# Performance work log

Hardware: AMD Instinct MI355X
Metric: run time of the kernel (lower is better)

Reference implementation:

```python
import jax, jax.numpy as jnp
import numpy as np

N_NODES = 62      # config.note_num (SEED EEG electrodes)
BATCH   = 1024    # graphs per batch
IN_CH   = 5
HID     = 64
OUT_CH  = 3
K_HOPS  = 2       # config.K


def setup_inputs() -> dict:
    key = jax.random.key(0)
    ks = jax.random.split(key, 8)
    total = BATCH * N_NODES
    x = jax.random.normal(ks[0], (total, IN_CH), dtype=jnp.float32)
    # fully-connected per-graph edge_index in row-major order (incl. self-loops),
    # matching edge_weight.reshape(-1).repeat(batch_size) in the torch code
    src = jnp.repeat(jnp.arange(N_NODES, dtype=jnp.int32), N_NODES)
    dst = jnp.tile(jnp.arange(N_NODES, dtype=jnp.int32), N_NODES)
    offs = (jnp.arange(BATCH, dtype=jnp.int32) * N_NODES)[:, None]
    edge_index = jnp.stack([
        (src[None, :] + offs).reshape(-1),
        (dst[None, :] + offs).reshape(-1),
    ])  # [2, BATCH*3844]
    batch = jnp.repeat(jnp.arange(BATCH, dtype=jnp.int32), N_NODES)
    n_tril = N_NODES * (N_NODES + 1) // 2  # 1953
    edge_weight_param = jax.random.normal(ks[1], (n_tril,), dtype=jnp.float32)
    w1 = jax.random.normal(ks[2], (HID, IN_CH), dtype=jnp.float32) * (1.0 / np.sqrt(IN_CH))
    b1 = jnp.zeros((HID,), dtype=jnp.float32)
    w2 = jax.random.normal(ks[3], (HID, HID), dtype=jnp.float32) * (1.0 / np.sqrt(HID))
    b2 = jnp.zeros((HID,), dtype=jnp.float32)
    wfc = jax.random.normal(ks[4], (OUT_CH, HID), dtype=jnp.float32) * (1.0 / np.sqrt(HID))
    bfc = jnp.zeros((OUT_CH,), dtype=jnp.float32)
    return dict(x=x, edge_index=edge_index, batch=batch,
                edge_weight_param=edge_weight_param,
                w1=w1, b1=b1, w2=w2, b2=b2, wfc=wfc, bfc=bfc)


def _gcn_norm(edge_index, edge_weight, num_nodes):
    # Graph already contains every self-loop, so add_remaining_self_loops only
    # reorders edges; normalization math is identical on the original edge set.
    row, col = edge_index[0], edge_index[1]
    deg = jax.ops.segment_sum(jnp.abs(edge_weight), row, num_segments=num_nodes)
    deg_inv_sqrt = jnp.where(deg > 0, jax.lax.rsqrt(deg), 0.0)
    return deg_inv_sqrt[row] * edge_weight * deg_inv_sqrt[col]


def _rsgconv(x, src, dst, norm, w, b):
    n = x.shape[0]
    for _ in range(K_HOPS):  # K propagation hops (gather-scale-scatter)
        x = jax.ops.segment_sum(norm[:, None] * x[src], dst, num_segments=n)
    return x @ w.T + b


def reference(x, edge_index, batch, edge_weight_param, w1, b1, w2, b2, wfc, bfc):
    num_nodes = x.shape[0]
    # rebuild symmetric dense 62x62 edge-weight matrix from learnable tril vector
    xs, ys = jnp.tril_indices(N_NODES)
    W = jnp.zeros((N_NODES, N_NODES), dtype=x.dtype).at[xs, ys].set(edge_weight_param)
    W = W + W.T - jnp.diag(jnp.diag(W))
    edge_weight = jnp.tile(W.reshape(-1), BATCH)  # [BATCH*3844]
    norm = _gcn_norm(edge_index, edge_weight, num_nodes)
    src, dst = edge_index[0], edge_index[1]
    h = jax.nn.relu(_rsgconv(x, src, dst, norm, w1, b1))
    h = jax.nn.relu(_rsgconv(h, src, dst, norm, w2, b2))
    pooled = jax.ops.segment_sum(h, batch, num_segments=BATCH)  # global_add_pool
    # dropout is identity in eval mode
    return pooled @ wfc.T + bfc
```

## Files before the change

kernel.cpp:

```cpp
#include <hip/hip_runtime.h>

#define NN 62
#define NP 64
#define NBATCH 1024
#define IN_CH 5
#define HID 64
#define OUT_CH 3
#define NTRIL 1953
#define H1S 72
#define GS 17
#define SAS 68

typedef _Float16 f16;
typedef f16 half8 __attribute__((ext_vector_type(8)));
typedef float floatx4 __attribute__((ext_vector_type(4)));

__global__ __launch_bounds__(256, 4) void graph_net(
    const float* __restrict__ x,
    const float* __restrict__ ewp,
    const float* __restrict__ w1, const float* __restrict__ b1,
    const float* __restrict__ w2, const float* __restrict__ b2,
    const float* __restrict__ wfc, const float* __restrict__ bfc,
    float* __restrict__ out) {
    __shared__ __align__(16) char smem[37120];
    f16* sAh = (f16*)smem;
    f16* sAl = (f16*)(smem + 9216);
    f16* sUTh = (f16*)smem;
    f16* sUTl = (f16*)(smem + 9216);
    float* sG = (float*)smem;
    float* sA = (float*)(smem + 18432);
    f16* sA2h = (f16*)(smem + 18432);
    f16* sA2l = (f16*)(smem + 27648);
    f16* sH1h = (f16*)(smem + 18432);
    f16* sH1l = (f16*)(smem + 27648);
    float* sDinv = (float*)(smem + 36864);
    float* sPool = (float*)(smem + 36864);

    const int t = threadIdx.x;
    const int lane = t & 63;
    const int w = __builtin_amdgcn_readfirstlane(t >> 6);
    const int g = blockIdx.x;
    const float* xg = x + (size_t)g * (NN * IN_CH);

    const int jn = lane & 15;
    const int qd = lane >> 4;
    const int jglob = 16 * w + jn;

    int xi[IN_CH];
    {
        const int L = (lane < NN) ? lane : (NN - 1);
        const int* xgi = (const int*)xg;
#pragma unroll
        for (int c = 0; c < IN_CH; ++c) xi[c] = xgi[L * IN_CH + c];
    }
    float w1r[IN_CH];
#pragma unroll
    for (int c = 0; c < IN_CH; ++c) w1r[c] = w1[lane * IN_CH + c];

#pragma unroll
    for (int k = 0; k < 8; ++k) {
        int i = t + 256 * k;
        if (i < NTRIL) {
            int r = (int)((sqrtf(8.f * (float)i + 1.f) - 1.f) * 0.5f);
            while (r * (r + 1) / 2 > i) --r;
            while ((r + 1) * (r + 2) / 2 <= i) ++r;
            int c = i - r * (r + 1) / 2;
            float v = ewp[i];
            sA[r * SAS + c] = v;
            sA[c * SAS + r] = v;
        }
    }
    __syncthreads();

    if (t < NN) {
        float s0 = 0.f, s1 = 0.f;
        for (int j = 0; j < NN; j += 2) {
            s0 += fabsf(sA[t * SAS + j]);
            s1 += fabsf(sA[t * SAS + j + 1]);
        }
        float s = s0 + s1;
        sDinv[t] = (s > 0.f) ? (1.0f / sqrtf(s)) : 0.f;
    }
    __syncthreads();

#pragma unroll
    for (int k = 0; k < 16; ++k) {
        int idx = t + 256 * k;
        int r = idx >> 6, c = idx & 63;
        float v = (r < NN && c < NN) ? sDinv[r] * sA[r * SAS + c] * sDinv[c] : 0.f;
        f16 vh = (f16)v;
        sAh[r * H1S + c] = vh;
        sAl[r * H1S + c] = (f16)(v - (float)vh);
    }
    __syncthreads();

    half8 bSh[2], bSl[2];
#pragma unroll
    for (int ks = 0; ks < 2; ++ks) {
        bSh[ks] = *(const half8*)(sAh + jglob * H1S + qd * 8 + 32 * ks);
        bSl[ks] = *(const half8*)(sAl + jglob * H1S + qd * 8 + 32 * ks);
    }
    floatx4 D2[4];
#pragma unroll
    for (int T = 0; T < 4; ++T) { D2[T][0]=0.f; D2[T][1]=0.f; D2[T][2]=0.f; D2[T][3]=0.f; }
#pragma unroll
    for (int T = 0; T < 4; ++T) {
#pragma unroll
        for (int ks = 0; ks < 2; ++ks) {
            const half8 ah = *(const half8*)(sAh + (16 * T + jn) * H1S + qd * 8 + 32 * ks);
            const half8 al = *(const half8*)(sAl + (16 * T + jn) * H1S + qd * 8 + 32 * ks);
            D2[T] = __builtin_amdgcn_mfma_f32_16x16x32_f16(al, bSh[ks], D2[T], 0, 0, 0);
            D2[T] = __builtin_amdgcn_mfma_f32_16x16x32_f16(ah, bSl[ks], D2[T], 0, 0, 0);
            D2[T] = __builtin_amdgcn_mfma_f32_16x16x32_f16(ah, bSh[ks], D2[T], 0, 0, 0);
        }
    }
#pragma unroll
    for (int T = 0; T < 4; ++T)
#pragma unroll
        for (int r = 0; r < 4; ++r) {
            const int n = 16 * T + qd * 4 + r;
            float v = D2[T][r];
            f16 vh = (f16)v;
            sA2h[n * H1S + jglob] = vh;
            sA2l[n * H1S + jglob] = (f16)(v - (float)vh);
        }
    __syncthreads();

    half8 aFh[4][2], aFl[4][2];
#pragma unroll
    for (int T = 0; T < 4; ++T)
#pragma unroll
        for (int ks = 0; ks < 2; ++ks) {
            aFh[T][ks] = *(const half8*)(sA2h + (16 * T + jn) * H1S + qd * 8 + 32 * ks);
            aFl[T][ks] = *(const half8*)(sA2l + (16 * T + jn) * H1S + qd * 8 + 32 * ks);
        }

#pragma unroll
    for (int ni = 0; ni < 16; ++ni) {
        const int n = 16 * w + ni;
        if (n < NN) {
            float u = 0.f;
#pragma unroll
            for (int c = 0; c < IN_CH; ++c)
                u += __int_as_float(__builtin_amdgcn_readlane(xi[c], n)) * w1r[c];
            f16 uh = (f16)u;
            sUTh[lane * H1S + n] = uh;
            sUTl[lane * H1S + n] = (f16)(u - (float)uh);
        }
    }
    if (t < 128) {
        const int n = 62 + (t >> 6);
        sUTh[(t & 63) * H1S + n] = (f16)0.f;
        sUTl[(t & 63) * H1S + n] = (f16)0.f;
    }
    __syncthreads();

    half8 bUh[2], bUl[2];
#pragma unroll
    for (int ks = 0; ks < 2; ++ks) {
        bUh[ks] = *(const half8*)(sUTh + jglob * H1S + qd * 8 + 32 * ks);
        bUl[ks] = *(const half8*)(sUTl + jglob * H1S + qd * 8 + 32 * ks);
    }
    floatx4 C1[4];
#pragma unroll
    for (int T = 0; T < 4; ++T) { C1[T][0]=0.f; C1[T][1]=0.f; C1[T][2]=0.f; C1[T][3]=0.f; }
#pragma unroll
    for (int T = 0; T < 4; ++T) {
#pragma unroll
        for (int ks = 0; ks < 2; ++ks) {
            C1[T] = __builtin_amdgcn_mfma_f32_16x16x32_f16(aFl[T][ks], bUh[ks], C1[T], 0, 0, 0);
            C1[T] = __builtin_amdgcn_mfma_f32_16x16x32_f16(aFh[T][ks], bUl[ks], C1[T], 0, 0, 0);
            C1[T] = __builtin_amdgcn_mfma_f32_16x16x32_f16(aFh[T][ks], bUh[ks], C1[T], 0, 0, 0);
        }
    }
    {
        const float b1r = b1[jglob];
#pragma unroll
        for (int T = 0; T < 4; ++T)
#pragma unroll
            for (int r = 0; r < 4; ++r) {
                const int n = 16 * T + qd * 4 + r;
                float v = fmaxf(C1[T][r] + b1r, 0.f);
                f16 vh = (f16)v;
                sH1h[n * H1S + jglob] = vh;
                sH1l[n * H1S + jglob] = (f16)(v - (float)vh);
            }
    }
    floatx4 w2lo[2], w2hi[2];
#pragma unroll
    for (int ks = 0; ks < 2; ++ks) {
        w2lo[ks] = *(const floatx4*)(w2 + jglob * HID + qd * 8 + 32 * ks);
        w2hi[ks] = *(const floatx4*)(w2 + jglob * HID + qd * 8 + 32 * ks + 4);
    }
    __syncthreads();

    half8 bWh[2], bWl[2];
#pragma unroll
    for (int ks = 0; ks < 2; ++ks)
#pragma unroll
        for (int i = 0; i < 4; ++i) {
            f16 h0 = (f16)w2lo[ks][i];
            bWh[ks][i] = h0;
            bWl[ks][i] = (f16)(w2lo[ks][i] - (float)h0);
            f16 h1 = (f16)w2hi[ks][i];
            bWh[ks][4 + i] = h1;
            bWl[ks][4 + i] = (f16)(w2hi[ks][i] - (float)h1);
        }
    floatx4 Cg[4];
#pragma unroll
    for (int T = 0; T < 4; ++T) { Cg[T][0]=0.f; Cg[T][1]=0.f; Cg[T][2]=0.f; Cg[T][3]=0.f; }
#pragma unroll
    for (int T = 0; T < 4; ++T) {
#pragma unroll
        for (int ks = 0; ks < 2; ++ks) {
            const half8 aH = *(const half8*)(sH1h + (16 * T + jn) * H1S + qd * 8 + 32 * ks);
            const half8 aL = *(const half8*)(sH1l + (16 * T + jn) * H1S + qd * 8 + 32 * ks);
            Cg[T] = __builtin_amdgcn_mfma_f32_16x16x32_f16(aL, bWh[ks], Cg[T], 0, 0, 0);
            Cg[T] = __builtin_amdgcn_mfma_f32_16x16x32_f16(aH, bWl[ks], Cg[T], 0, 0, 0);
            Cg[T] = __builtin_amdgcn_mfma_f32_16x16x32_f16(aH, bWh[ks], Cg[T], 0, 0, 0);
        }
    }
    {
        float* gw = sG + w * (NP * GS);
#pragma unroll
        for (int T = 0; T < 4; ++T)
#pragma unroll
            for (int r = 0; r < 4; ++r)
                gw[(16 * T + qd * 4 + r) * GS + jn] = Cg[T][r];
    }

    half8 bGh[2], bGl[2];
    {
        const float* gr = sG + w * (NP * GS);
#pragma unroll
        for (int ks = 0; ks < 2; ++ks)
#pragma unroll
            for (int i = 0; i < 8; ++i) {
                float v = gr[(qd * 8 + i + 32 * ks) * GS + jn];
                f16 vh = (f16)v;
                bGh[ks][i] = vh;
                bGl[ks][i] = (f16)(v - (float)vh);
            }
    }

    floatx4 C2[4];
#pragma unroll
    for (int T = 0; T < 4; ++T) { C2[T][0]=0.f; C2[T][1]=0.f; C2[T][2]=0.f; C2[T][3]=0.f; }
#pragma unroll
    for (int T = 0; T < 4; ++T) {
#pragma unroll
        for (int ks = 0; ks < 2; ++ks) {
            C2[T] = __builtin_amdgcn_mfma_f32_16x16x32_f16(aFl[T][ks], bGh[ks], C2[T], 0, 0, 0);
            C2[T] = __builtin_amdgcn_mfma_f32_16x16x32_f16(aFh[T][ks], bGl[ks], C2[T], 0, 0, 0);
            C2[T] = __builtin_amdgcn_mfma_f32_16x16x32_f16(aFh[T][ks], bGh[ks], C2[T], 0, 0, 0);
        }
    }

    {
        const float b2r = b2[jglob];
        float pool = 0.f;
#pragma unroll
        for (int T = 0; T < 4; ++T)
#pragma unroll
            for (int r = 0; r < 4; ++r) {
                const int n = 16 * T + qd * 4 + r;
                float v = fmaxf(C2[T][r] + b2r, 0.f);
                pool += (n < NN) ? v : 0.f;
            }
        pool += __shfl_xor(pool, 16);
        pool += __shfl_xor(pool, 32);
        if (lane < 16) sPool[jglob] = pool;
    }
    __syncthreads();

    if (t < HID) {
        const float pv = sPool[t];
#pragma unroll
        for (int o = 0; o < OUT_CH; ++o) {
            float vv = pv * wfc[o * HID + t];
            vv += __shfl_xor(vv, 1);
            vv += __shfl_xor(vv, 2);
            vv += __shfl_xor(vv, 4);
            vv += __shfl_xor(vv, 8);
            vv += __shfl_xor(vv, 16);
            vv += __shfl_xor(vv, 32);
            if (t == 0) out[g * OUT_CH + o] = vv + bfc[o];
        }
    }
}

extern "C" void kernel_launch(void* const* d_in, const int* in_sizes, int n_in,
                              void* d_out, int out_size, void* d_ws, size_t ws_size,
                              hipStream_t stream) {
    const float* x   = (const float*)d_in[0];
    const float* ewp = (const float*)d_in[3];
    const float* w1  = (const float*)d_in[4];
    const float* b1  = (const float*)d_in[5];
    const float* w2  = (const float*)d_in[6];
    const float* b2  = (const float*)d_in[7];
    const float* wfc = (const float*)d_in[8];
    const float* bfc = (const float*)d_in[9];
    float* out = (float*)d_out;
    (void)d_ws; (void)ws_size;

    graph_net<<<NBATCH, 256, 0, stream>>>(x, ewp, w1, b1, w2, b2, wfc, bfc, out);
}
```

Before: 107.3 us.

## Build layer-1 U fragments directly in registers and parallelize degree sums

Stages the graph's node features in shared memory, and each lane computes its own MFMA B-fragment of x·W1ᵀ straight into registers. This replaces the readlane loop, the shared-memory transpose of U and one block barrier. The degree computation is split across four threads per row with vectorized loads and a shuffle reduction, in place of one serial thread per row. It re-maps the shared-memory regions (H1 and G are relocated) and grows shared usage slightly, which could affect occupancy at four blocks per CU.

```diff
diff --git a/kernel.cpp b/kernel.cpp
--- a/kernel.cpp
+++ b/kernel.cpp
@@ -10,6 +10,7 @@
 #define H1S 72
 #define GS 17
 #define SAS 68
+#define XS 8
 
 typedef _Float16 f16;
 typedef f16 half8 __attribute__((ext_vector_type(8)));
@@ -22,40 +23,41 @@
     const float* __restrict__ w2, const float* __restrict__ b2,
     const float* __restrict__ wfc, const float* __restrict__ bfc,
     float* __restrict__ out) {
-    __shared__ __align__(16) char smem[37120];
+    __shared__ __align__(16) char smem[39168];
     f16* sAh = (f16*)smem;
     f16* sAl = (f16*)(smem + 9216);
-    f16* sUTh = (f16*)smem;
-    f16* sUTl = (f16*)(smem + 9216);
-    float* sG = (float*)smem;
+    f16* sH1h = (f16*)smem;
+    f16* sH1l = (f16*)(smem + 9216);
     float* sA = (float*)(smem + 18432);
     f16* sA2h = (f16*)(smem + 18432);
     f16* sA2l = (f16*)(smem + 27648);
-    f16* sH1h = (f16*)(smem + 18432);
-    f16* sH1l = (f16*)(smem + 27648);
+    float* sG = (float*)(smem + 18432);
     float* sDinv = (float*)(smem + 36864);
     float* sPool = (float*)(smem + 36864);
+    float* sX = (float*)(smem + 37120);
 
     const int t = threadIdx.x;
     const int lane = t & 63;
     const int w = __builtin_amdgcn_readfirstlane(t >> 6);
     const int g = blockIdx.x;
-    const float* xg = x + (size_t)g * (NN * IN_CH);
 
     const int jn = lane & 15;
     const int qd = lane >> 4;
     const int jglob = 16 * w + jn;
 
-    int xi[IN_CH];
-    {
-        const int L = (lane < NN) ? lane : (NN - 1);
-        const int* xgi = (const int*)xg;
-#pragma unroll
-        for (int c = 0; c < IN_CH; ++c) xi[c] = xgi[L * IN_CH + c];
-    }
     float w1r[IN_CH];
 #pragma unroll
-    for (int c = 0; c < IN_CH; ++c) w1r[c] = w1[lane * IN_CH + c];
+    for (int c = 0; c < IN_CH; ++c) w1r[c] = w1[jglob * IN_CH + c];
+
+    if (t < 64) {
+        const int* xgi = (const int*)(x + (size_t)g * (NN * IN_CH));
+        const int L = (t < NN) ? t : 0;
+#pragma unroll
+        for (int c = 0; c < IN_CH; ++c) {
+            int v = (t < NN) ? xgi[L * IN_CH + c] : 0;
+            ((int*)sX)[t * XS + c] = v;
+        }
+    }
 
 #pragma unroll
     for (int k = 0; k < 8; ++k) {
@@ -72,15 +74,42 @@
     }
     __syncthreads();
 
-    if (t < NN) {
-        float s0 = 0.f, s1 = 0.f;
-        for (int j = 0; j < NN; j += 2) {
-            s0 += fabsf(sA[t * SAS + j]);
-            s1 += fabsf(sA[t * SAS + j + 1]);
-        }
-        float s = s0 + s1;
-        sDinv[t] = (s > 0.f) ? (1.0f / sqrtf(s)) : 0.f;
-    }
+    if (t < 4 * NN) {
+        const int row = t >> 2, part = t & 3;
+        const float* rp = sA + row * SAS + part * 16;
+        float s = 0.f;
+        if (part < 3) {
+#pragma unroll
+            for (int q = 0; q < 4; ++q) {
+                floatx4 v = *(const floatx4*)(rp + 4 * q);
+                s += fabsf(v[0]) + fabsf(v[1]) + fabsf(v[2]) + fabsf(v[3]);
+            }
+        } else {
+#pragma unroll
+            for (int q = 0; q < 3; ++q) {
+                floatx4 v = *(const floatx4*)(rp + 4 * q);
+                s += fabsf(v[0]) + fabsf(v[1]) + fabsf(v[2]) + fabsf(v[3]);
+            }
+            s += fabsf(rp[12]) + fabsf(rp[13]);
+        }
+        s += __shfl_xor(s, 1);
+        s += __shfl_xor(s, 2);
+        if (part == 0) sDinv[row] = (s > 0.f) ? (1.0f / sqrtf(s)) : 0.f;
+    }
+
+    half8 bUh[2], bUl[2];
+#pragma unroll
+    for (int ks = 0; ks < 2; ++ks)
+#pragma unroll
+        for (int i = 0; i < 8; ++i) {
+            const float* xr = sX + (qd * 8 + i + 32 * ks) * XS;
+            floatx4 xv = *(const floatx4*)xr;
+            float u = xv[0] * w1r[0] + xv[1] * w1r[1] + xv[2] * w1r[2]
+                    + xv[3] * w1r[3] + xr[4] * w1r[4];
+            f16 uh = (f16)u;
+            bUh[ks][i] = uh;
+            bUl[ks][i] = (f16)(u - (float)uh);
+        }
     __syncthreads();
 
 #pragma unroll
@@ -135,32 +164,6 @@
             aFl[T][ks] = *(const half8*)(sA2l + (16 * T + jn) * H1S + qd * 8 + 32 * ks);
         }
 
-#pragma unroll
-    for (int ni = 0; ni < 16; ++ni) {
-        const int n = 16 * w + ni;
-        if (n < NN) {
-            float u = 0.f;
-#pragma unroll
-            for (int c = 0; c < IN_CH; ++c)
-                u += __int_as_float(__builtin_amdgcn_readlane(xi[c], n)) * w1r[c];
-            f16 uh = (f16)u;
-            sUTh[lane * H1S + n] = uh;
-            sUTl[lane * H1S + n] = (f16)(u - (float)uh);
-        }
-    }
-    if (t < 128) {
-        const int n = 62 + (t >> 6);
-        sUTh[(t & 63) * H1S + n] = (f16)0.f;
-        sUTl[(t & 63) * H1S + n] = (f16)0.f;
-    }
-    __syncthreads();
-
-    half8 bUh[2], bUl[2];
-#pragma unroll
-    for (int ks = 0; ks < 2; ++ks) {
-        bUh[ks] = *(const half8*)(sUTh + jglob * H1S + qd * 8 + 32 * ks);
-        bUl[ks] = *(const half8*)(sUTl + jglob * H1S + qd * 8 + 32 * ks);
-    }
     floatx4 C1[4];
 #pragma unroll
     for (int T = 0; T < 4; ++T) { C1[T][0]=0.f; C1[T][1]=0.f; C1[T][2]=0.f; C1[T][3]=0.f; }
```

After: 105.7 us. No clear change (-1.5%).
